# Kernel optimization log

Measured on AMD Instinct MI355X. Metric: run time of the kernel, lower is better.

Reference implementation:

```python
import jax, jax.numpy as jnp
import numpy as np

B, D, L = 4096, 128, 4
ALPHA = 1.0
SLOPE = 0.1  # LeakyReLU negative slope


def _leaky(h):
    return jnp.where(h > 0, h, SLOPE * h)


def _dleaky(h):
    return jnp.where(h > 0, 1.0, SLOPE).astype(h.dtype)


def setup_inputs() -> dict:
    key = jax.random.key(0)
    ks = jax.random.split(key, 7)
    scale = 0.5 / np.sqrt(D)  # keep residual roughly Lipschitz < 1
    x = jax.random.normal(ks[0], (B, D), jnp.float32)
    W1 = jax.random.normal(ks[1], (L, D, D), jnp.float32) * scale
    b1 = jax.random.normal(ks[2], (L, D), jnp.float32) * 0.01
    W2 = jax.random.normal(ks[3], (L, D, D), jnp.float32) * scale
    b2 = jax.random.normal(ks[4], (L, D), jnp.float32) * 0.01
    W3 = jax.random.normal(ks[5], (L, D, D), jnp.float32) * scale
    b3 = jax.random.normal(ks[6], (L, D), jnp.float32) * 0.01
    return {"x": x, "W1": W1, "b1": b1, "W2": W2, "b2": b2, "W3": W3, "b3": b3}


def reference(x, W1, b1, W2, b2, W3, b3):
    logdet = jnp.zeros(x.shape[0], x.dtype)
    for i in range(L):  # small fixed number of structurally distinct blocks
        w1, w2, w3 = W1[i], W2[i], W3[i]
        # --- block forward: x <- x + alpha * f(x) ---
        h1 = x @ w1.T + b1[i]
        h2 = _leaky(h1) @ w2.T + b2[i]
        f = _leaky(h2) @ w3.T + b3[i]
        x = x + ALPHA * f
        # --- log|det J_f| evaluated at the NEW x (as in the original code) ---
        g1 = x @ w1.T + b1[i]          # [B, D] pre-activation 1
        d1 = _dleaky(g1)
        g2 = _leaky(g1) @ w2.T + b2[i]  # [B, D] pre-activation 2
        d2 = _dleaky(g2)
        # J[b] = w3 @ diag(d2[b]) @ w2 @ diag(d1[b]) @ w1  -> [B, D, D]
        J = (w3[None, :, :] * d2[:, None, :]) @ w2
        J = (J * d1[:, None, :]) @ w1
        s = jnp.linalg.svd(J, compute_uv=False)  # [B, D] singular values
        logdet = logdet + jnp.sum(jnp.log(s), axis=-1)
    return x, logdet
```

## Files before the change

### kernel.cpp

```cpp
#include <hip/hip_runtime.h>

typedef __attribute__((ext_vector_type(8))) short short8;
typedef __attribute__((ext_vector_type(4))) float float4f;

#define PITCH 136
#define ROWS 32
#define LOG_SLOPE -2.302585092994046f
#define LN2 0.6931471805599453f
#define NBLK 140
#define LDS_BYTES 69760
#define WS_BIAS 4160
#define WS_WPLANES 8192
#define NWELEM 196608

__device__ __forceinline__ float bf2f(unsigned int u) {
    return __builtin_bit_cast(float, u << 16);
}
__device__ __forceinline__ unsigned short f2bf(float f) {
    unsigned int x = __builtin_bit_cast(unsigned int, f);
    x += 0x7fff + ((x >> 16) & 1);
    return (unsigned short)(x >> 16);
}
__device__ __forceinline__ float4f vmsub(float4f a, float s, float4f b) {
    a[0] -= s * b[0]; a[1] -= s * b[1]; a[2] -= s * b[2]; a[3] -= s * b[3];
    return a;
}

template<int ISF32>
__device__ __forceinline__ float ldv(const void* p, int i) {
    if (ISF32) return ((const float*)p)[i];
    return bf2f(((const unsigned short*)p)[i]);
}

__device__ __forceinline__ int detect_f32(const unsigned short* W1u, int lane) {
    unsigned int u = W1u[lane * 2];
    unsigned int e = (u >> 7) & 0xFF;
    int bad = (e < 64) || (e > 135);
    return __ballot(bad) != 0ull;
}

__device__ __forceinline__ float4f mfma16(short8 a, short8 b, float4f c) {
    return __builtin_amdgcn_mfma_f32_16x16x32_bf16(a, b, c, 0, 0, 0);
}

__device__ __forceinline__ void split8(float4f a, float4f b, short8& hi, short8& lo) {
#pragma unroll
    for (int j = 0; j < 4; ++j) {
        float v = a[j]; unsigned short h = f2bf(v);
        hi[j] = (short)h; lo[j] = (short)f2bf(v - bf2f(h));
        v = b[j]; h = f2bf(v);
        hi[4 + j] = (short)h; lo[4 + j] = (short)f2bf(v - bf2f(h));
    }
}

__global__ void k_prep(const void* __restrict__ W1, const void* __restrict__ W2,
                       const void* __restrict__ W3, const void* __restrict__ b1,
                       const void* __restrict__ b2, const void* __restrict__ b3,
                       float* __restrict__ ws) {
    const int tid = threadIdx.x, bid = blockIdx.x;
    const int isf32 = detect_f32((const unsigned short*)W1, tid & 63);
    unsigned short* whi = (unsigned short*)(ws + WS_WPLANES);
    unsigned short* wlo = whi + NWELEM;
    if (bid < 96) {
        int s = (bid * 256 + tid) * 8;
        int mat = s >> 14, off = s & 16383;
        int wsel = mat >> 2;
        const void* Wm = wsel == 0 ? W1 : (wsel == 1 ? W2 : W3);
        int src = (mat & 3) * 16384 + off;
        short8 hi, lo;
        if (isf32) {
            const float* p = (const float*)Wm + src;
            split8(*(const float4f*)p, *(const float4f*)(p + 4), hi, lo);
        } else {
            hi = *(const short8*)((const unsigned short*)Wm + src);
            lo = (short8){0, 0, 0, 0, 0, 0, 0, 0};
        }
        *(short8*)(whi + s) = hi;
        *(short8*)(wlo + s) = lo;
    } else {
        for (int e = tid; e < 1536; e += 256) {
            int bsel = e >> 9, idx = e & 511;
            const void* bp = bsel == 0 ? b1 : (bsel == 1 ? b2 : b3);
            ws[WS_BIAS + e] = isf32 ? ((const float*)bp)[idx]
                                    : bf2f(((const unsigned short*)bp)[idx]);
        }
        if (tid == 0) ((int*)ws)[0] = 0;
    }
}

struct W8 { short8 v[16]; };

__device__ __forceinline__ W8 loadW(const unsigned short* __restrict__ wh,
                                    const unsigned short* __restrict__ wl,
                                    int c0, int c1, int q) {
    W8 r;
#pragma unroll
    for (int kk = 0; kk < 4; ++kk) {
        const int kc = kk * 32 + q * 8;
        r.v[kk * 4 + 0] = *(const short8*)(wh + c0 * 128 + kc);
        r.v[kk * 4 + 1] = *(const short8*)(wh + c1 * 128 + kc);
        r.v[kk * 4 + 2] = *(const short8*)(wl + c0 * 128 + kc);
        r.v[kk * 4 + 3] = *(const short8*)(wl + c1 * 128 + kc);
    }
    return r;
}

template<int MODE>
__device__ __forceinline__ W8 matvec(const W8& w,
        const unsigned short* inh, const unsigned short* inl,
        unsigned short* outh, unsigned short* outl,
        const unsigned short* resh, const unsigned short* resl,
        const unsigned short* __restrict__ nwh, const unsigned short* __restrict__ nwl,
        const float* __restrict__ bias,
        int lane, int colb, int* cnt) {
    const int m = lane & 15, q = lane >> 4;
    const int c0 = colb + m, c1 = colb + 16 + m;
    float b0 = bias[c0], b1v = bias[c1];
    float4f acc[2][2];
#pragma unroll
    for (int rt = 0; rt < 2; ++rt) {
        acc[rt][0] = (float4f){b0, b0, b0, b0};
        acc[rt][1] = (float4f){b1v, b1v, b1v, b1v};
    }
    __syncthreads();
    W8 wn = loadW(nwh, nwl, c0, c1, q);
#pragma unroll
    for (int kk = 0; kk < 4; ++kk) {
        const int kc = kk * 32 + q * 8;
#pragma unroll
        for (int rt = 0; rt < 2; ++rt) {
            short8 xh = *(const short8*)(inh + (rt * 16 + m) * PITCH + kc);
            short8 xl = *(const short8*)(inl + (rt * 16 + m) * PITCH + kc);
            acc[rt][0] = mfma16(xh, w.v[kk * 4 + 0], acc[rt][0]);
            acc[rt][0] = mfma16(xl, w.v[kk * 4 + 0], acc[rt][0]);
            acc[rt][0] = mfma16(xh, w.v[kk * 4 + 2], acc[rt][0]);
            acc[rt][1] = mfma16(xh, w.v[kk * 4 + 1], acc[rt][1]);
            acc[rt][1] = mfma16(xl, w.v[kk * 4 + 1], acc[rt][1]);
            acc[rt][1] = mfma16(xh, w.v[kk * 4 + 3], acc[rt][1]);
        }
    }
    int c[2][4];
#pragma unroll
    for (int rt = 0; rt < 2; ++rt) {
#pragma unroll
        for (int r = 0; r < 4; ++r) {
            float v0 = acc[rt][0][r], v1 = acc[rt][1][r];
            int row = rt * 16 + q * 4 + r;
            int o0 = row * PITCH + c0, o1 = row * PITCH + c1;
            if (MODE == 1) {
                v0 += bf2f(resh[o0]) + bf2f(resl[o0]);
                v1 += bf2f(resh[o1]) + bf2f(resl[o1]);
            }
            if (MODE >= 2) c[rt][r] = (v0 <= 0.0f) + (v1 <= 0.0f);
            if (MODE == 0 || MODE == 2) {
                v0 = v0 > 0.0f ? v0 : 0.1f * v0;
                v1 = v1 > 0.0f ? v1 : 0.1f * v1;
            }
            if (MODE != 3) {
                unsigned short h0 = f2bf(v0);
                outh[o0] = h0; outl[o0] = f2bf(v0 - bf2f(h0));
                unsigned short h1 = f2bf(v1);
                outh[o1] = h1; outl[o1] = f2bf(v1 - bf2f(h1));
            }
        }
    }
    if (MODE >= 2) {
#pragma unroll
        for (int rt = 0; rt < 2; ++rt) {
#pragma unroll
            for (int r = 0; r < 4; ++r) {
                int cc = c[rt][r];
                cc += __shfl_xor(cc, 1);
                cc += __shfl_xor(cc, 2);
                cc += __shfl_xor(cc, 4);
                cc += __shfl_xor(cc, 8);
                if (m == 0) atomicAdd(&cnt[rt * 16 + q * 4 + r], cc);
            }
        }
    }
    return wn;
}

template<int ISF32>
__device__ __forceinline__ void fwd(int bid, int tid, int lane, char* ldsb,
                                    const void* x, const float* ws, void* out,
                                    float* wsw) {
    unsigned short* P = (unsigned short*)ldsb;
    unsigned short* Ah = P;
    unsigned short* Al = P + 1 * ROWS * PITCH;
    unsigned short* Bh = P + 2 * ROWS * PITCH;
    unsigned short* Bl = P + 3 * ROWS * PITCH;
    unsigned short* Th = P + 4 * ROWS * PITCH;
    unsigned short* Tl = P + 5 * ROWS * PITCH;
    unsigned short* Uh = P + 6 * ROWS * PITCH;
    unsigned short* Ul = P + 7 * ROWS * PITCH;
    int* cnt = (int*)(P + 8 * ROWS * PITCH);
    const unsigned short* whi = (const unsigned short*)(ws + WS_WPLANES);
    const unsigned short* wlo = whi + NWELEM;
    const float* bias = ws + WS_BIAS;
    const int r0 = bid * ROWS;
    const int m = lane & 15, q = lane >> 4;
    const int colb = (tid >> 6) * 32;
    const int c0 = colb + m, c1 = colb + 16 + m;
    W8 wcur = loadW(whi, wlo, c0, c1, q);
    for (int e = tid; e < ROWS * 128; e += 256) {
        int r = e >> 7, c = e & 127;
        float v = ldv<ISF32>(x, (r0 + r) * 128 + c);
        unsigned short h = f2bf(v);
        Ah[r * PITCH + c] = h;
        Al[r * PITCH + c] = f2bf(v - bf2f(h));
    }
    if (tid < ROWS) cnt[tid] = 0;
    unsigned short *curh = Ah, *curl = Al, *othh = Bh, *othl = Bl;
#pragma unroll 1
    for (int layer = 0; layer < 4; ++layer) {
        const unsigned short* w1h = whi + (0 + layer) * 16384;
        const unsigned short* w1l = wlo + (0 + layer) * 16384;
        const unsigned short* w2h = whi + (4 + layer) * 16384;
        const unsigned short* w2l = wlo + (4 + layer) * 16384;
        const unsigned short* w3h = whi + (8 + layer) * 16384;
        const unsigned short* w3l = wlo + (8 + layer) * 16384;
        const unsigned short* n1h = whi + ((layer + 1) & 3) * 16384;
        const unsigned short* n1l = wlo + ((layer + 1) & 3) * 16384;
        const float* b1p = bias + layer * 128;
        const float* b2p = bias + 512 + layer * 128;
        const float* b3p = bias + 1024 + layer * 128;
        wcur = matvec<0>(wcur, curh, curl, Th, Tl, 0, 0, w2h, w2l, b1p, lane, colb, cnt);
        wcur = matvec<0>(wcur, Th, Tl, Uh, Ul, 0, 0, w3h, w3l, b2p, lane, colb, cnt);
        wcur = matvec<1>(wcur, Uh, Ul, othh, othl, curh, curl, w1h, w1l, b3p, lane, colb, cnt);
        wcur = matvec<2>(wcur, othh, othl, Th, Tl, 0, 0, w2h, w2l, b1p, lane, colb, cnt);
        wcur = matvec<3>(wcur, Th, Tl, Th, Tl, 0, 0, n1h, n1l, b2p, lane, colb, cnt);
        unsigned short* t;
        t = curh; curh = othh; othh = t;
        t = curl; curl = othl; othl = t;
    }
    __syncthreads();
    for (int e = tid; e < ROWS * 128; e += 256) {
        int r = e >> 7, c = e & 127;
        float v = bf2f(curh[r * PITCH + c]) + bf2f(curl[r * PITCH + c]);
        if (ISF32) ((float*)out)[(r0 + r) * 128 + c] = v;
        else ((unsigned short*)out)[(r0 + r) * 128 + c] = f2bf(v);
    }
    if (tid < ROWS) wsw[64 + r0 + tid] = (float)cnt[tid];
}

template<int ISF32>
__device__ __forceinline__ float lu_logdet(int id, int tid, float* lds,
        const void* W1, const void* W2, const void* W3) {
    const int wsel = id % 3;
    const void* Wm = (wsel == 0 ? W1 : (wsel == 1 ? W2 : W3));
    const int ofs = (id / 3) * 16384;
    const int tx = tid & 31, ty = tid >> 5;
    float* rowbuf = lds;
    float* colbuf = lds + 1024;
    float4f V[16];
#pragma unroll
    for (int m = 0; m < 16; ++m) {
        int base = ofs + (ty + 8 * m) * 128 + 4 * tx;
        if (ISF32) {
            V[m] = *(const float4f*)((const float*)Wm + base);
        } else {
            ushort4 u = *(const ushort4*)((const unsigned short*)Wm + base);
            V[m] = (float4f){bf2f(u.x), bf2f(u.y), bf2f(u.z), bf2f(u.w)};
        }
    }
    if (ty < 4) *(float4f*)&rowbuf[ty * 128 + 4 * tx] = V[0];
    if (tx == 0) {
#pragma unroll
        for (int j = 0; j < 4; ++j) {
#pragma unroll
            for (int mg = 0; mg < 4; ++mg) {
                float4f t = {V[mg * 4 + 0][j], V[mg * 4 + 1][j],
                             V[mg * 4 + 2][j], V[mg * 4 + 3][j]};
                *(float4f*)&colbuf[j * 128 + ty * 16 + mg * 4] = t;
            }
        }
    }
    __syncthreads();
    float logacc = 0.0f;
#pragma unroll 1
    for (int kap = 0; kap < 32; ++kap) {
        const int K = kap * 4;
        const int buf = (kap & 1) * 512;
        float4f D[4], R[4], C[4][4];
#pragma unroll
        for (int j = 0; j < 4; ++j) {
            D[j] = *(const float4f*)&rowbuf[buf + j * 128 + K];
            R[j] = *(const float4f*)&rowbuf[buf + j * 128 + 4 * tx];
#pragma unroll
            for (int mg = 0; mg < 4; ++mg)
                C[j][mg] = *(const float4f*)&colbuf[buf + j * 128 + ty * 16 + mg * 4];
        }
        float p0 = D[0][0], i0 = 1.0f / p0;
        float l10 = D[1][0] * i0, l20 = D[2][0] * i0, l30 = D[3][0] * i0;
        D[1] = vmsub(D[1], l10, D[0]); R[1] = vmsub(R[1], l10, R[0]);
        D[2] = vmsub(D[2], l20, D[0]); R[2] = vmsub(R[2], l20, R[0]);
        D[3] = vmsub(D[3], l30, D[0]); R[3] = vmsub(R[3], l30, R[0]);
        float p1 = D[1][1], i1 = 1.0f / p1;
        float l21 = D[2][1] * i1, l31 = D[3][1] * i1;
        D[2] = vmsub(D[2], l21, D[1]); R[2] = vmsub(R[2], l21, R[1]);
        D[3] = vmsub(D[3], l31, D[1]); R[3] = vmsub(R[3], l31, R[1]);
        float p2 = D[2][2], i2 = 1.0f / p2;
        float l32 = D[3][2] * i2;
        D[3] = vmsub(D[3], l32, D[2]); R[3] = vmsub(R[3], l32, R[2]);
        float p3 = D[3][3], i3 = 1.0f / p3;
        logacc += __log2f(fabsf(p0)) + __log2f(fabsf(p1))
                + __log2f(fabsf(p2)) + __log2f(fabsf(p3));
        float iv[4] = {i0, i1, i2, i3};
#pragma unroll
        for (int i = 0; i < 4; ++i) {
#pragma unroll
            for (int mg = 0; mg < 4; ++mg) {
#pragma unroll
                for (int e = 0; e < 4; ++e) {
                    int r = ty + 32 * mg + 8 * e;
                    C[i][mg][e] = (r > K + i) ? C[i][mg][e] * iv[i] : 0.0f;
                }
            }
#pragma unroll
            for (int j = i + 1; j < 4; ++j) {
                float uij = D[i][j];
#pragma unroll
                for (int mg = 0; mg < 4; ++mg)
                    C[j][mg] = vmsub(C[j][mg], uij, C[i][mg]);
            }
        }
#pragma unroll
        for (int mg = 0; mg < 4; ++mg) {
#pragma unroll
            for (int e = 0; e < 4; ++e) {
                float4f v = V[mg * 4 + e];
                v = vmsub(v, C[0][mg][e], R[0]);
                v = vmsub(v, C[1][mg][e], R[1]);
                v = vmsub(v, C[2][mg][e], R[2]);
                v = vmsub(v, C[3][mg][e], R[3]);
                V[mg * 4 + e] = v;
            }
        }
        if (kap < 31) {
            const int nbuf = ((kap + 1) & 1) * 512;
            const int tb = (kap & 1) ? 0 : 4;
            const int mn = (kap + 1) >> 1;
            if (ty >= tb && ty < tb + 4) {
                float4f val;
                switch (mn) {
                case 0:  val = V[0];  break; case 1:  val = V[1];  break;
                case 2:  val = V[2];  break; case 3:  val = V[3];  break;
                case 4:  val = V[4];  break; case 5:  val = V[5];  break;
                case 6:  val = V[6];  break; case 7:  val = V[7];  break;
                case 8:  val = V[8];  break; case 9:  val = V[9];  break;
                case 10: val = V[10]; break; case 11: val = V[11]; break;
                case 12: val = V[12]; break; case 13: val = V[13]; break;
                case 14: val = V[14]; break; default: val = V[15]; break;
                }
                *(float4f*)&rowbuf[nbuf + (ty - tb) * 128 + 4 * tx] = val;
            }
            if (tx == kap + 1) {
#pragma unroll
                for (int j = 0; j < 4; ++j) {
#pragma unroll
                    for (int mg = 0; mg < 4; ++mg) {
                        float4f t = {V[mg * 4 + 0][j], V[mg * 4 + 1][j],
                                     V[mg * 4 + 2][j], V[mg * 4 + 3][j]};
                        *(float4f*)&colbuf[nbuf + j * 128 + ty * 16 + mg * 4] = t;
                    }
                }
            }
        }
        __syncthreads();
    }
    return logacc * LN2;
}

__global__ __launch_bounds__(256) void k_main(
        const void* __restrict__ x,
        const void* __restrict__ W1, const void* __restrict__ b1,
        const void* __restrict__ W2, const void* __restrict__ b2,
        const void* __restrict__ W3, const void* __restrict__ b3,
        void* __restrict__ out, float* __restrict__ ws) {
    extern __shared__ __align__(16) char ldsb[];
    __shared__ int s_last;
    const int tid = threadIdx.x;
    const int lane = tid & 63;
    const int isf32 = detect_f32((const unsigned short*)W1, lane);

    if (blockIdx.x < 12) {
        float ld = isf32 ? lu_logdet<1>(blockIdx.x, tid, (float*)ldsb, W1, W2, W3)
                         : lu_logdet<0>(blockIdx.x, tid, (float*)ldsb, W1, W2, W3);
        if (tid == 0) ws[2 + blockIdx.x] = ld;
    } else {
        const int bid = blockIdx.x - 12;
        if (isf32) fwd<1>(bid, tid, lane, ldsb, x, ws, out, ws);
        else       fwd<0>(bid, tid, lane, ldsb, x, ws, out, ws);
    }

    __threadfence();
    if (tid == 0) s_last = (atomicAdd((int*)ws, 1) == NBLK - 1);
    __syncthreads();
    if (!s_last) return;
    __threadfence();
    float s = 0.0f;
#pragma unroll
    for (int i = 0; i < 12; ++i) s += ws[2 + i];
    for (int b = tid; b < 4096; b += 256) {
        float v = s + LOG_SLOPE * ws[64 + b];
        if (isf32) ((float*)out)[524288 + b] = v;
        else ((unsigned short*)out)[524288 + b] = f2bf(v);
    }
}

extern "C" void kernel_launch(void* const* d_in, const int* in_sizes, int n_in,
                              void* d_out, int out_size, void* d_ws, size_t ws_size,
                              hipStream_t stream) {
    const void* x  = d_in[0];
    const void* W1 = d_in[1];
    const void* b1 = d_in[2];
    const void* W2 = d_in[3];
    const void* b2 = d_in[4];
    const void* W3 = d_in[5];
    const void* b3 = d_in[6];
    float* ws = (float*)d_ws;

    hipLaunchKernelGGL(k_prep, dim3(97), dim3(256), 0, stream,
                       W1, W2, W3, b1, b2, b3, ws);
    hipLaunchKernelGGL(k_main, dim3(NBLK), dim3(256), LDS_BYTES, stream,
                       x, W1, b1, W2, b2, W3, b3, d_out, ws);
}
```

Baseline: 136.5 us.

## Fuse weight hi/lo split into main kernel and drop prep kernel

Measured after the change: 147.9 us. 8.3% more time.

```diff
diff --git a/kernel.cpp b/kernel.cpp
--- a/kernel.cpp
+++ b/kernel.cpp
@@ -9,9 +9,6 @@
 #define LN2 0.6931471805599453f
 #define NBLK 140
 #define LDS_BYTES 69760
-#define WS_BIAS 4160
-#define WS_WPLANES 8192
-#define NWELEM 196608
 
 __device__ __forceinline__ float bf2f(unsigned int u) {
     return __builtin_bit_cast(float, u << 16);
@@ -53,69 +50,84 @@
     }
 }
 
-__global__ void k_prep(const void* __restrict__ W1, const void* __restrict__ W2,
-                       const void* __restrict__ W3, const void* __restrict__ b1,
-                       const void* __restrict__ b2, const void* __restrict__ b3,
-                       float* __restrict__ ws) {
-    const int tid = threadIdx.x, bid = blockIdx.x;
-    const int isf32 = detect_f32((const unsigned short*)W1, tid & 63);
-    unsigned short* whi = (unsigned short*)(ws + WS_WPLANES);
-    unsigned short* wlo = whi + NWELEM;
-    if (bid < 96) {
-        int s = (bid * 256 + tid) * 8;
-        int mat = s >> 14, off = s & 16383;
-        int wsel = mat >> 2;
-        const void* Wm = wsel == 0 ? W1 : (wsel == 1 ? W2 : W3);
-        int src = (mat & 3) * 16384 + off;
-        short8 hi, lo;
-        if (isf32) {
-            const float* p = (const float*)Wm + src;
-            split8(*(const float4f*)p, *(const float4f*)(p + 4), hi, lo);
-        } else {
-            hi = *(const short8*)((const unsigned short*)Wm + src);
-            lo = (short8){0, 0, 0, 0, 0, 0, 0, 0};
-        }
-        *(short8*)(whi + s) = hi;
-        *(short8*)(wlo + s) = lo;
-    } else {
-        for (int e = tid; e < 1536; e += 256) {
-            int bsel = e >> 9, idx = e & 511;
-            const void* bp = bsel == 0 ? b1 : (bsel == 1 ? b2 : b3);
-            ws[WS_BIAS + e] = isf32 ? ((const float*)bp)[idx]
-                                    : bf2f(((const unsigned short*)bp)[idx]);
-        }
-        if (tid == 0) ((int*)ws)[0] = 0;
-    }
-}
-
 struct W8 { short8 v[16]; };
-
-__device__ __forceinline__ W8 loadW(const unsigned short* __restrict__ wh,
-                                    const unsigned short* __restrict__ wl,
-                                    int c0, int c1, int q) {
-    W8 r;
+template<int ISF32> struct WRaw;
+template<> struct WRaw<1> { float4f v[16]; };
+template<> struct WRaw<0> { short8 v[8];  };
+
+template<int ISF32>
+__device__ __forceinline__ WRaw<ISF32> loadRaw(const void* W, int c0, int c1, int q);
+template<>
+__device__ __forceinline__ WRaw<1> loadRaw<1>(const void* W, int c0, int c1, int q) {
+    WRaw<1> r;
+    const float* p = (const float*)W;
 #pragma unroll
     for (int kk = 0; kk < 4; ++kk) {
         const int kc = kk * 32 + q * 8;
-        r.v[kk * 4 + 0] = *(const short8*)(wh + c0 * 128 + kc);
-        r.v[kk * 4 + 1] = *(const short8*)(wh + c1 * 128 + kc);
-        r.v[kk * 4 + 2] = *(const short8*)(wl + c0 * 128 + kc);
-        r.v[kk * 4 + 3] = *(const short8*)(wl + c1 * 128 + kc);
+        r.v[kk * 4 + 0] = *(const float4f*)(p + c0 * 128 + kc);
+        r.v[kk * 4 + 1] = *(const float4f*)(p + c0 * 128 + kc + 4);
+        r.v[kk * 4 + 2] = *(const float4f*)(p + c1 * 128 + kc);
+        r.v[kk * 4 + 3] = *(const float4f*)(p + c1 * 128 + kc + 4);
     }
     return r;
 }
-
-template<int MODE>
+template<>
+__device__ __forceinline__ WRaw<0> loadRaw<0>(const void* W, int c0, int c1, int q) {
+    WRaw<0> r;
+    const unsigned short* p = (const unsigned short*)W;
+#pragma unroll
+    for (int kk = 0; kk < 4; ++kk) {
+        const int kc = kk * 32 + q * 8;
+        r.v[kk * 2 + 0] = *(const short8*)(p + c0 * 128 + kc);
+        r.v[kk * 2 + 1] = *(const short8*)(p + c1 * 128 + kc);
+    }
+    return r;
+}
+
+template<int ISF32>
+__device__ __forceinline__ W8 convertW(const WRaw<ISF32>& raw);
+template<>
+__device__ __forceinline__ W8 convertW<1>(const WRaw<1>& raw) {
+    W8 w;
+#pragma unroll
+    for (int kk = 0; kk < 4; ++kk) {
+        split8(raw.v[kk * 4 + 0], raw.v[kk * 4 + 1], w.v[kk * 4 + 0], w.v[kk * 4 + 2]);
+        split8(raw.v[kk * 4 + 2], raw.v[kk * 4 + 3], w.v[kk * 4 + 1], w.v[kk * 4 + 3]);
+    }
+    return w;
+}
+template<>
+__device__ __forceinline__ W8 convertW<0>(const WRaw<0>& raw) {
+    W8 w;
+    const short8 z = {0, 0, 0, 0, 0, 0, 0, 0};
+#pragma unroll
+    for (int kk = 0; kk < 4; ++kk) {
+        w.v[kk * 4 + 0] = raw.v[kk * 2 + 0];
+        w.v[kk * 4 + 1] = raw.v[kk * 2 + 1];
+        w.v[kk * 4 + 2] = z;
+        w.v[kk * 4 + 3] = z;
+    }
+    return w;
+}
+
+template<int ISF32>
+__device__ __forceinline__ const void* wptr(const void* W, int ofs) {
+    return ISF32 ? (const void*)((const float*)W + ofs)
+                 : (const void*)((const unsigned short*)W + ofs);
+}
+
+template<int MODE, int ISF32>
 __device__ __forceinline__ W8 matvec(const W8& w,
         const unsigned short* inh, const unsigned short* inl,
         unsigned short* outh, unsigned short* outl,
         const unsigned short* resh, const unsigned short* resl,
-        const unsigned short* __restrict__ nwh, const unsigned short* __restrict__ nwl,
-        const float* __restrict__ bias,
+        const void* __restrict__ nw,
+        const void* __restrict__ bias, int bofs,
         int lane, int colb, int* cnt) {
     const int m = lane & 15, q = lane >> 4;
     const int c0 = colb + m, c1 = colb + 16 + m;
-    float b0 = bias[c0], b1v = bias[c1];
+    float b0 = ldv<ISF32>(bias, bofs + c0);
+    float b1v = ldv<ISF32>(bias, bofs + c1);
     float4f acc[2][2];
 #pragma unroll
     for (int rt = 0; rt < 2; ++rt) {
@@ -123,7 +135,7 @@
         acc[rt][1] = (float4f){b1v, b1v, b1v, b1v};
     }
     __syncthreads();
-    W8 wn = loadW(nwh, nwl, c0, c1, q);
+    WRaw<ISF32> raw = loadRaw<ISF32>(nw, c0, c1, q);
 #pragma unroll
     for (int kk = 0; kk < 4; ++kk) {
         const int kc = kk * 32 + q * 8;
@@ -139,6 +151,7 @@
             acc[rt][1] = mfma16(xh, w.v[kk * 4 + 3], acc[rt][1]);
         }
     }
+    W8 wn = convertW<ISF32>(raw);
     int c[2][4];
 #pragma unroll
     for (int rt = 0; rt < 2; ++rt) {
@@ -183,8 +196,8 @@
 
 template<int ISF32>
 __device__ __forceinline__ void fwd(int bid, int tid, int lane, char* ldsb,
-                                    const void* x, const float* ws, void* out,
-                                    float* wsw) {
+        const void* x, const void* W1, const void* b1, const void* W2,
+        const void* b2, const void* W3, const void* b3, void* out, float* wsw) {
     unsigned short* P = (unsigned short*)ldsb;
     unsigned short* Ah = P;
     unsigned short* Al = P + 1 * ROWS * PITCH;
@@ -195,14 +208,11 @@
     unsigned short* Uh = P + 6 * ROWS * PITCH;
     unsigned short* Ul = P + 7 * ROWS * PITCH;
     int* cnt = (int*)(P + 8 * ROWS * PITCH);
-    const unsigned short* whi = (const unsigned short*)(ws + WS_WPLANES);
-    const unsigned short* wlo = whi + NWELEM;
-    const float* bias = ws + WS_BIAS;
     const int r0 = bid * ROWS;
     const int m = lane & 15, q = lane >> 4;
     const int colb = (tid >> 6) * 32;
     const int c0 = colb + m, c1 = colb + 16 + m;
-    W8 wcur = loadW(whi, wlo, c0, c1, q);
+    WRaw<ISF32> raw0 = loadRaw<ISF32>(W1, c0, c1, q);
     for (int e = tid; e < ROWS * 128; e += 256) {
         int r = e >> 7, c = e & 127;
         float v = ldv<ISF32>(x, (r0 + r) * 128 + c);
@@ -211,25 +221,20 @@
         Al[r * PITCH + c] = f2bf(v - bf2f(h));
     }
     if (tid < ROWS) cnt[tid] = 0;
+    W8 wcur = convertW<ISF32>(raw0);
     unsigned short *curh = Ah, *curl = Al, *othh = Bh, *othl = Bl;
 #pragma unroll 1
     for (int layer = 0; layer < 4; ++layer) {
-        const unsigned short* w1h = whi + (0 + layer) * 16384;
-        const unsigned short* w1l = wlo + (0 + layer) * 16384;
-        const unsigned short* w2h = whi + (4 + layer) * 16384;
-        const unsigned short* w2l = wlo + (4 + layer) * 16384;
-        const unsigned short* w3h = whi + (8 + layer) * 16384;
-        const unsigned short* w3l = wlo + (8 + layer) * 16384;
-        const unsigned short* n1h = whi + ((layer + 1) & 3) * 16384;
-        const unsigned short* n1l = wlo + ((layer + 1) & 3) * 16384;
-        const float* b1p = bias + layer * 128;
-        const float* b2p = bias + 512 + layer * 128;
-        const float* b3p = bias + 1024 + layer * 128;
-        wcur = matvec<0>(wcur, curh, curl, Th, Tl, 0, 0, w2h, w2l, b1p, lane, colb, cnt);
-        wcur = matvec<0>(wcur, Th, Tl, Uh, Ul, 0, 0, w3h, w3l, b2p, lane, colb, cnt);
-        wcur = matvec<1>(wcur, Uh, Ul, othh, othl, curh, curl, w1h, w1l, b3p, lane, colb, cnt);
-        wcur = matvec<2>(wcur, othh, othl, Th, Tl, 0, 0, w2h, w2l, b1p, lane, colb, cnt);
-        wcur = matvec<3>(wcur, Th, Tl, Th, Tl, 0, 0, n1h, n1l, b2p, lane, colb, cnt);
+        const int wofs = layer * 16384, bofs = layer * 128;
+        const void* w1p = wptr<ISF32>(W1, wofs);
+        const void* w2p = wptr<ISF32>(W2, wofs);
+        const void* w3p = wptr<ISF32>(W3, wofs);
+        const void* n1p = wptr<ISF32>(W1, ((layer + 1) & 3) * 16384);
+        wcur = matvec<0, ISF32>(wcur, curh, curl, Th, Tl, 0, 0, w2p, b1, bofs, lane, colb, cnt);
+        wcur = matvec<0, ISF32>(wcur, Th, Tl, Uh, Ul, 0, 0, w3p, b2, bofs, lane, colb, cnt);
+        wcur = matvec<1, ISF32>(wcur, Uh, Ul, othh, othl, curh, curl, w1p, b3, bofs, lane, colb, cnt);
+        wcur = matvec<2, ISF32>(wcur, othh, othl, Th, Tl, 0, 0, w2p, b1, bofs, lane, colb, cnt);
+        wcur = matvec<3, ISF32>(wcur, Th, Tl, Th, Tl, 0, 0, n1p, b2, bofs, lane, colb, cnt);
         unsigned short* t;
         t = curh; curh = othh; othh = t;
         t = curl; curl = othl; othl = t;
@@ -372,7 +377,7 @@
     return logacc * LN2;
 }
 
-__global__ __launch_bounds__(256) void k_main(
+__global__ __launch_bounds__(256, 1) void k_main(
         const void* __restrict__ x,
         const void* __restrict__ W1, const void* __restrict__ b1,
         const void* __restrict__ W2, const void* __restrict__ b2,
@@ -390,8 +395,8 @@
         if (tid == 0) ws[2 + blockIdx.x] = ld;
     } else {
         const int bid = blockIdx.x - 12;
-        if (isf32) fwd<1>(bid, tid, lane, ldsb, x, ws, out, ws);
-        else       fwd<0>(bid, tid, lane, ldsb, x, ws, out, ws);
+        if (isf32) fwd<1>(bid, tid, lane, ldsb, x, W1, b1, W2, b2, W3, b3, out, ws);
+        else       fwd<0>(bid, tid, lane, ldsb, x, W1, b1, W2, b2, W3, b3, out, ws);
     }
 
     __threadfence();
@@ -421,8 +426,7 @@
     const void* b3 = d_in[6];
     float* ws = (float*)d_ws;
 
-    hipLaunchKernelGGL(k_prep, dim3(97), dim3(256), 0, stream,
-                       W1, W2, W3, b1, b2, b3, ws);
+    hipMemsetAsync(d_ws, 0, 8, stream);
     hipLaunchKernelGGL(k_main, dim3(NBLK), dim3(256), LDS_BYTES, stream,
                        x, W1, b1, W2, b2, W3, b3, d_out, ws);
 }
```

## Widen blocked LU panel from 4 to 8 columns in logdet path

Applied to the files above, without the earlier changes.

Result: slower. 146.2 us (+7.1%).

```diff
diff --git a/kernel.cpp b/kernel.cpp
--- a/kernel.cpp
+++ b/kernel.cpp
@@ -252,7 +252,7 @@
     const int ofs = (id / 3) * 16384;
     const int tx = tid & 31, ty = tid >> 5;
     float* rowbuf = lds;
-    float* colbuf = lds + 1024;
+    float* colbuf = lds + 2048;
     float4f V[16];
 #pragma unroll
     for (int m = 0; m < 16; ++m) {
@@ -264,51 +264,51 @@
             V[m] = (float4f){bf2f(u.x), bf2f(u.y), bf2f(u.z), bf2f(u.w)};
         }
     }
-    if (ty < 4) *(float4f*)&rowbuf[ty * 128 + 4 * tx] = V[0];
-    if (tx == 0) {
-#pragma unroll
-        for (int j = 0; j < 4; ++j) {
+    *(float4f*)&rowbuf[ty * 128 + 4 * tx] = V[0];
+    if (tx < 2) {
+#pragma unroll
+        for (int j0 = 0; j0 < 4; ++j0) {
 #pragma unroll
             for (int mg = 0; mg < 4; ++mg) {
-                float4f t = {V[mg * 4 + 0][j], V[mg * 4 + 1][j],
-                             V[mg * 4 + 2][j], V[mg * 4 + 3][j]};
-                *(float4f*)&colbuf[j * 128 + ty * 16 + mg * 4] = t;
+                float4f t = {V[mg * 4 + 0][j0], V[mg * 4 + 1][j0],
+                             V[mg * 4 + 2][j0], V[mg * 4 + 3][j0]};
+                *(float4f*)&colbuf[(tx * 4 + j0) * 128 + ty * 16 + mg * 4] = t;
             }
         }
     }
     __syncthreads();
     float logacc = 0.0f;
 #pragma unroll 1
-    for (int kap = 0; kap < 32; ++kap) {
-        const int K = kap * 4;
-        const int buf = (kap & 1) * 512;
-        float4f D[4], R[4], C[4][4];
-#pragma unroll
-        for (int j = 0; j < 4; ++j) {
-            D[j] = *(const float4f*)&rowbuf[buf + j * 128 + K];
+    for (int kap = 0; kap < 16; ++kap) {
+        const int K = kap * 8;
+        const int buf = (kap & 1) * 1024;
+        float4f D[8][2], R[8], C[8][4];
+#pragma unroll
+        for (int j = 0; j < 8; ++j) {
+            D[j][0] = *(const float4f*)&rowbuf[buf + j * 128 + K];
+            D[j][1] = *(const float4f*)&rowbuf[buf + j * 128 + K + 4];
             R[j] = *(const float4f*)&rowbuf[buf + j * 128 + 4 * tx];
 #pragma unroll
             for (int mg = 0; mg < 4; ++mg)
                 C[j][mg] = *(const float4f*)&colbuf[buf + j * 128 + ty * 16 + mg * 4];
         }
-        float p0 = D[0][0], i0 = 1.0f / p0;
-        float l10 = D[1][0] * i0, l20 = D[2][0] * i0, l30 = D[3][0] * i0;
-        D[1] = vmsub(D[1], l10, D[0]); R[1] = vmsub(R[1], l10, R[0]);
-        D[2] = vmsub(D[2], l20, D[0]); R[2] = vmsub(R[2], l20, R[0]);
-        D[3] = vmsub(D[3], l30, D[0]); R[3] = vmsub(R[3], l30, R[0]);
-        float p1 = D[1][1], i1 = 1.0f / p1;
-        float l21 = D[2][1] * i1, l31 = D[3][1] * i1;
-        D[2] = vmsub(D[2], l21, D[1]); R[2] = vmsub(R[2], l21, R[1]);
-        D[3] = vmsub(D[3], l31, D[1]); R[3] = vmsub(R[3], l31, R[1]);
-        float p2 = D[2][2], i2 = 1.0f / p2;
-        float l32 = D[3][2] * i2;
-        D[3] = vmsub(D[3], l32, D[2]); R[3] = vmsub(R[3], l32, R[2]);
-        float p3 = D[3][3], i3 = 1.0f / p3;
-        logacc += __log2f(fabsf(p0)) + __log2f(fabsf(p1))
-                + __log2f(fabsf(p2)) + __log2f(fabsf(p3));
-        float iv[4] = {i0, i1, i2, i3};
-#pragma unroll
-        for (int i = 0; i < 4; ++i) {
+        float iv[8];
+#pragma unroll
+        for (int i = 0; i < 8; ++i) {
+            float pi = D[i][i >> 2][i & 3];
+            float ivi = 1.0f / pi;
+            iv[i] = ivi;
+            logacc += __log2f(fabsf(pi));
+#pragma unroll
+            for (int j = i + 1; j < 8; ++j) {
+                float l = D[j][i >> 2][i & 3] * ivi;
+                D[j][0] = vmsub(D[j][0], l, D[i][0]);
+                D[j][1] = vmsub(D[j][1], l, D[i][1]);
+                R[j] = vmsub(R[j], l, R[i]);
+            }
+        }
+#pragma unroll
+        for (int i = 0; i < 8; ++i) {
 #pragma unroll
             for (int mg = 0; mg < 4; ++mg) {
 #pragma unroll
@@ -318,8 +318,8 @@
                 }
             }
 #pragma unroll
-            for (int j = i + 1; j < 4; ++j) {
-                float uij = D[i][j];
+            for (int j = i + 1; j < 8; ++j) {
+                float uij = D[i][j >> 2][j & 3];
 #pragma unroll
                 for (int mg = 0; mg < 4; ++mg)
                     C[j][mg] = vmsub(C[j][mg], uij, C[i][mg]);
@@ -330,39 +330,36 @@
 #pragma unroll
             for (int e = 0; e < 4; ++e) {
                 float4f v = V[mg * 4 + e];
-                v = vmsub(v, C[0][mg][e], R[0]);
-                v = vmsub(v, C[1][mg][e], R[1]);
-                v = vmsub(v, C[2][mg][e], R[2]);
-                v = vmsub(v, C[3][mg][e], R[3]);
+#pragma unroll
+                for (int i = 0; i < 8; ++i)
+                    v = vmsub(v, C[i][mg][e], R[i]);
                 V[mg * 4 + e] = v;
             }
         }
-        if (kap < 31) {
-            const int nbuf = ((kap + 1) & 1) * 512;
-            const int tb = (kap & 1) ? 0 : 4;
-            const int mn = (kap + 1) >> 1;
-            if (ty >= tb && ty < tb + 4) {
-                float4f val;
-                switch (mn) {
-                case 0:  val = V[0];  break; case 1:  val = V[1];  break;
-                case 2:  val = V[2];  break; case 3:  val = V[3];  break;
-                case 4:  val = V[4];  break; case 5:  val = V[5];  break;
-                case 6:  val = V[6];  break; case 7:  val = V[7];  break;
-                case 8:  val = V[8];  break; case 9:  val = V[9];  break;
-                case 10: val = V[10]; break; case 11: val = V[11]; break;
-                case 12: val = V[12]; break; case 13: val = V[13]; break;
-                case 14: val = V[14]; break; default: val = V[15]; break;
-                }
-                *(float4f*)&rowbuf[nbuf + (ty - tb) * 128 + 4 * tx] = val;
-            }
-            if (tx == kap + 1) {
-#pragma unroll
-                for (int j = 0; j < 4; ++j) {
+        if (kap < 15) {
+            const int nbuf = ((kap + 1) & 1) * 1024;
+            float4f val;
+            switch (kap + 1) {
+            case 1:  val = V[1];  break; case 2:  val = V[2];  break;
+            case 3:  val = V[3];  break; case 4:  val = V[4];  break;
+            case 5:  val = V[5];  break; case 6:  val = V[6];  break;
+            case 7:  val = V[7];  break; case 8:  val = V[8];  break;
+            case 9:  val = V[9];  break; case 10: val = V[10]; break;
+            case 11: val = V[11]; break; case 12: val = V[12]; break;
+            case 13: val = V[13]; break; case 14: val = V[14]; break;
+            default: val = V[15]; break;
+            }
+            *(float4f*)&rowbuf[nbuf + ty * 128 + 4 * tx] = val;
+            const int txb = 2 * (kap + 1);
+            if (tx == txb || tx == txb + 1) {
+                const int jb = (tx - txb) * 4;
+#pragma unroll
+                for (int j0 = 0; j0 < 4; ++j0) {
 #pragma unroll
                     for (int mg = 0; mg < 4; ++mg) {
-                        float4f t = {V[mg * 4 + 0][j], V[mg * 4 + 1][j],
-                                     V[mg * 4 + 2][j], V[mg * 4 + 3][j]};
-                        *(float4f*)&colbuf[nbuf + j * 128 + ty * 16 + mg * 4] = t;
+                        float4f t = {V[mg * 4 + 0][j0], V[mg * 4 + 1][j0],
+                                     V[mg * 4 + 2][j0], V[mg * 4 + 3][j0]};
+                        *(float4f*)&colbuf[nbuf + (jb + j0) * 128 + ty * 16 + mg * 4] = t;
                     }
                 }
             }
@@ -372,7 +369,7 @@
     return logacc * LN2;
 }
 
-__global__ __launch_bounds__(256) void k_main(
+__global__ __launch_bounds__(256, 1) void k_main(
         const void* __restrict__ x,
         const void* __restrict__ W1, const void* __restrict__ b1,
         const void* __restrict__ W2, const void* __restrict__ b2,
```

## Double block size to 512 threads, halving per-thread work in matvec and LU

Applied to the files above, without the earlier changes.

After: 140.8 us. 1.03x slower.

```diff
diff --git a/kernel.cpp b/kernel.cpp
--- a/kernel.cpp
+++ b/kernel.cpp
@@ -5,6 +5,7 @@
 
 #define PITCH 136
 #define ROWS 32
+#define THREADS 512
 #define LOG_SLOPE -2.302585092994046f
 #define LN2 0.6931471805599453f
 #define NBLK 140
@@ -88,25 +89,23 @@
     }
 }
 
-struct W8 { short8 v[16]; };
-
-__device__ __forceinline__ W8 loadW(const unsigned short* __restrict__ wh,
-                                    const unsigned short* __restrict__ wl,
-                                    int c0, int c1, int q) {
-    W8 r;
+struct W4 { short8 v[8]; };
+
+__device__ __forceinline__ W4 loadW4(const unsigned short* __restrict__ wh,
+                                     const unsigned short* __restrict__ wl,
+                                     int c0, int q) {
+    W4 r;
 #pragma unroll
     for (int kk = 0; kk < 4; ++kk) {
         const int kc = kk * 32 + q * 8;
-        r.v[kk * 4 + 0] = *(const short8*)(wh + c0 * 128 + kc);
-        r.v[kk * 4 + 1] = *(const short8*)(wh + c1 * 128 + kc);
-        r.v[kk * 4 + 2] = *(const short8*)(wl + c0 * 128 + kc);
-        r.v[kk * 4 + 3] = *(const short8*)(wl + c1 * 128 + kc);
+        r.v[kk * 2 + 0] = *(const short8*)(wh + c0 * 128 + kc);
+        r.v[kk * 2 + 1] = *(const short8*)(wl + c0 * 128 + kc);
     }
     return r;
 }
 
 template<int MODE>
-__device__ __forceinline__ W8 matvec(const W8& w,
+__device__ __forceinline__ W4 matvec(const W4& w,
         const unsigned short* inh, const unsigned short* inl,
         unsigned short* outh, unsigned short* outl,
         const unsigned short* resh, const unsigned short* resl,
@@ -114,53 +113,40 @@
         const float* __restrict__ bias,
         int lane, int colb, int* cnt) {
     const int m = lane & 15, q = lane >> 4;
-    const int c0 = colb + m, c1 = colb + 16 + m;
-    float b0 = bias[c0], b1v = bias[c1];
-    float4f acc[2][2];
-#pragma unroll
-    for (int rt = 0; rt < 2; ++rt) {
-        acc[rt][0] = (float4f){b0, b0, b0, b0};
-        acc[rt][1] = (float4f){b1v, b1v, b1v, b1v};
-    }
+    const int c0 = colb + m;
+    float b0 = bias[c0];
+    float4f acc0 = {b0, b0, b0, b0};
+    float4f acc1 = {b0, b0, b0, b0};
     __syncthreads();
-    W8 wn = loadW(nwh, nwl, c0, c1, q);
+    W4 wn = loadW4(nwh, nwl, c0, q);
 #pragma unroll
     for (int kk = 0; kk < 4; ++kk) {
         const int kc = kk * 32 + q * 8;
-#pragma unroll
-        for (int rt = 0; rt < 2; ++rt) {
-            short8 xh = *(const short8*)(inh + (rt * 16 + m) * PITCH + kc);
-            short8 xl = *(const short8*)(inl + (rt * 16 + m) * PITCH + kc);
-            acc[rt][0] = mfma16(xh, w.v[kk * 4 + 0], acc[rt][0]);
-            acc[rt][0] = mfma16(xl, w.v[kk * 4 + 0], acc[rt][0]);
-            acc[rt][0] = mfma16(xh, w.v[kk * 4 + 2], acc[rt][0]);
-            acc[rt][1] = mfma16(xh, w.v[kk * 4 + 1], acc[rt][1]);
-            acc[rt][1] = mfma16(xl, w.v[kk * 4 + 1], acc[rt][1]);
-            acc[rt][1] = mfma16(xh, w.v[kk * 4 + 3], acc[rt][1]);
-        }
+        short8 x0h = *(const short8*)(inh + m * PITCH + kc);
+        short8 x0l = *(const short8*)(inl + m * PITCH + kc);
+        short8 x1h = *(const short8*)(inh + (16 + m) * PITCH + kc);
+        short8 x1l = *(const short8*)(inl + (16 + m) * PITCH + kc);
+        acc0 = mfma16(x0h, w.v[kk * 2 + 0], acc0);
+        acc0 = mfma16(x0l, w.v[kk * 2 + 0], acc0);
+        acc0 = mfma16(x0h, w.v[kk * 2 + 1], acc0);
+        acc1 = mfma16(x1h, w.v[kk * 2 + 0], acc1);
+        acc1 = mfma16(x1l, w.v[kk * 2 + 0], acc1);
+        acc1 = mfma16(x1h, w.v[kk * 2 + 1], acc1);
     }
     int c[2][4];
 #pragma unroll
     for (int rt = 0; rt < 2; ++rt) {
 #pragma unroll
         for (int r = 0; r < 4; ++r) {
-            float v0 = acc[rt][0][r], v1 = acc[rt][1][r];
+            float v0 = rt == 0 ? acc0[r] : acc1[r];
             int row = rt * 16 + q * 4 + r;
-            int o0 = row * PITCH + c0, o1 = row * PITCH + c1;
-            if (MODE == 1) {
-                v0 += bf2f(resh[o0]) + bf2f(resl[o0]);
-                v1 += bf2f(resh[o1]) + bf2f(resl[o1]);
-            }
-            if (MODE >= 2) c[rt][r] = (v0 <= 0.0f) + (v1 <= 0.0f);
-            if (MODE == 0 || MODE == 2) {
-                v0 = v0 > 0.0f ? v0 : 0.1f * v0;
-                v1 = v1 > 0.0f ? v1 : 0.1f * v1;
-            }
+            int o0 = row * PITCH + c0;
+            if (MODE == 1) v0 += bf2f(resh[o0]) + bf2f(resl[o0]);
+            if (MODE >= 2) c[rt][r] = (v0 <= 0.0f);
+            if (MODE == 0 || MODE == 2) v0 = v0 > 0.0f ? v0 : 0.1f * v0;
             if (MODE != 3) {
                 unsigned short h0 = f2bf(v0);
                 outh[o0] = h0; outl[o0] = f2bf(v0 - bf2f(h0));
-                unsigned short h1 = f2bf(v1);
-                outh[o1] = h1; outl[o1] = f2bf(v1 - bf2f(h1));
             }
         }
     }
@@ -200,10 +186,10 @@
     const float* bias = ws + WS_BIAS;
     const int r0 = bid * ROWS;
     const int m = lane & 15, q = lane >> 4;
-    const int colb = (tid >> 6) * 32;
-    const int c0 = colb + m, c1 = colb + 16 + m;
-    W8 wcur = loadW(whi, wlo, c0, c1, q);
-    for (int e = tid; e < ROWS * 128; e += 256) {
+    const int colb = (tid >> 6) * 16;
+    const int c0 = colb + m;
+    W4 wcur = loadW4(whi, wlo, c0, q);
+    for (int e = tid; e < ROWS * 128; e += THREADS) {
         int r = e >> 7, c = e & 127;
         float v = ldv<ISF32>(x, (r0 + r) * 128 + c);
         unsigned short h = f2bf(v);
@@ -235,7 +221,7 @@
         t = curl; curl = othl; othl = t;
     }
     __syncthreads();
-    for (int e = tid; e < ROWS * 128; e += 256) {
+    for (int e = tid; e < ROWS * 128; e += THREADS) {
         int r = e >> 7, c = e & 127;
         float v = bf2f(curh[r * PITCH + c]) + bf2f(curl[r * PITCH + c]);
         if (ISF32) ((float*)out)[(r0 + r) * 128 + c] = v;
@@ -253,10 +239,10 @@
     const int tx = tid & 31, ty = tid >> 5;
     float* rowbuf = lds;
     float* colbuf = lds + 1024;
-    float4f V[16];
-#pragma unroll
-    for (int m = 0; m < 16; ++m) {
-        int base = ofs + (ty + 8 * m) * 128 + 4 * tx;
+    float4f V[8];
+#pragma unroll
+    for (int m = 0; m < 8; ++m) {
+        int base = ofs + (ty + 16 * m) * 128 + 4 * tx;
         if (ISF32) {
             V[m] = *(const float4f*)((const float*)Wm + base);
         } else {
@@ -268,12 +254,10 @@
     if (tx == 0) {
 #pragma unroll
         for (int j = 0; j < 4; ++j) {
-#pragma unroll
-            for (int mg = 0; mg < 4; ++mg) {
-                float4f t = {V[mg * 4 + 0][j], V[mg * 4 + 1][j],
-                             V[mg * 4 + 2][j], V[mg * 4 + 3][j]};
-                *(float4f*)&colbuf[j * 128 + ty * 16 + mg * 4] = t;
-            }
+            float4f t0 = {V[0][j], V[1][j], V[2][j], V[3][j]};
+            float4f t1 = {V[4][j], V[5][j], V[6][j], V[7][j]};
+            *(float4f*)&colbuf[j * 128 + ty * 8] = t0;
+            *(float4f*)&colbuf[j * 128 + ty * 8 + 4] = t1;
         }
     }
     __syncthreads();
@@ -282,14 +266,13 @@
     for (int kap = 0; kap < 32; ++kap) {
         const int K = kap * 4;
         const int buf = (kap & 1) * 512;
-        float4f D[4], R[4], C[4][4];
+        float4f D[4], R[4], C[4][2];
 #pragma unroll
         for (int j = 0; j < 4; ++j) {
             D[j] = *(const float4f*)&rowbuf[buf + j * 128 + K];
             R[j] = *(const float4f*)&rowbuf[buf + j * 128 + 4 * tx];
-#pragma unroll
-            for (int mg = 0; mg < 4; ++mg)
-                C[j][mg] = *(const float4f*)&colbuf[buf + j * 128 + ty * 16 + mg * 4];
+            C[j][0] = *(const float4f*)&colbuf[buf + j * 128 + ty * 8];
+            C[j][1] = *(const float4f*)&colbuf[buf + j * 128 + ty * 8 + 4];
         }
         float p0 = D[0][0], i0 = 1.0f / p0;
         float l10 = D[1][0] * i0, l20 = D[2][0] * i0, l30 = D[3][0] * i0;
@@ -310,60 +293,49 @@
 #pragma unroll
         for (int i = 0; i < 4; ++i) {
 #pragma unroll
-            for (int mg = 0; mg < 4; ++mg) {
+            for (int cg = 0; cg < 2; ++cg) {
 #pragma unroll
                 for (int e = 0; e < 4; ++e) {
-                    int r = ty + 32 * mg + 8 * e;
-                    C[i][mg][e] = (r > K + i) ? C[i][mg][e] * iv[i] : 0.0f;
+                    int r = ty + 16 * (cg * 4 + e);
+                    C[i][cg][e] = (r > K + i) ? C[i][cg][e] * iv[i] : 0.0f;
                 }
             }
 #pragma unroll
             for (int j = i + 1; j < 4; ++j) {
                 float uij = D[i][j];
-#pragma unroll
-                for (int mg = 0; mg < 4; ++mg)
-                    C[j][mg] = vmsub(C[j][mg], uij, C[i][mg]);
-            }
-        }
-#pragma unroll
-        for (int mg = 0; mg < 4; ++mg) {
-#pragma unroll
-            for (int e = 0; e < 4; ++e) {
-                float4f v = V[mg * 4 + e];
-                v = vmsub(v, C[0][mg][e], R[0]);
-                v = vmsub(v, C[1][mg][e], R[1]);
-                v = vmsub(v, C[2][mg][e], R[2]);
-                v = vmsub(v, C[3][mg][e], R[3]);
-                V[mg * 4 + e] = v;
-            }
+                C[j][0] = vmsub(C[j][0], uij, C[i][0]);
+                C[j][1] = vmsub(C[j][1], uij, C[i][1]);
+            }
+        }
+#pragma unroll
+        for (int m = 0; m < 8; ++m) {
+            float4f v = V[m];
+            v = vmsub(v, C[0][m >> 2][m & 3], R[0]);
+            v = vmsub(v, C[1][m >> 2][m & 3], R[1]);
+            v = vmsub(v, C[2][m >> 2][m & 3], R[2]);
+            v = vmsub(v, C[3][m >> 2][m & 3], R[3]);
+            V[m] = v;
         }
         if (kap < 31) {
+            const int nk = K + 4;
             const int nbuf = ((kap + 1) & 1) * 512;
-            const int tb = (kap & 1) ? 0 : 4;
-            const int mn = (kap + 1) >> 1;
-            if (ty >= tb && ty < tb + 4) {
+            if ((ty >> 2) == ((nk & 15) >> 2)) {
                 float4f val;
-                switch (mn) {
-                case 0:  val = V[0];  break; case 1:  val = V[1];  break;
-                case 2:  val = V[2];  break; case 3:  val = V[3];  break;
-                case 4:  val = V[4];  break; case 5:  val = V[5];  break;
-                case 6:  val = V[6];  break; case 7:  val = V[7];  break;
-                case 8:  val = V[8];  break; case 9:  val = V[9];  break;
-                case 10: val = V[10]; break; case 11: val = V[11]; break;
-                case 12: val = V[12]; break; case 13: val = V[13]; break;
-                case 14: val = V[14]; break; default: val = V[15]; break;
+                switch (nk >> 4) {
+                case 0:  val = V[0]; break; case 1:  val = V[1]; break;
+                case 2:  val = V[2]; break; case 3:  val = V[3]; break;
+                case 4:  val = V[4]; break; case 5:  val = V[5]; break;
+                case 6:  val = V[6]; break; default: val = V[7]; break;
                 }
-                *(float4f*)&rowbuf[nbuf + (ty - tb) * 128 + 4 * tx] = val;
-            }
-            if (tx == kap + 1) {
+                *(float4f*)&rowbuf[nbuf + (ty & 3) * 128 + 4 * tx] = val;
+            }
+            if (tx == (nk >> 2)) {
 #pragma unroll
                 for (int j = 0; j < 4; ++j) {
-#pragma unroll
-                    for (int mg = 0; mg < 4; ++mg) {
-                        float4f t = {V[mg * 4 + 0][j], V[mg * 4 + 1][j],
-                                     V[mg * 4 + 2][j], V[mg * 4 + 3][j]};
-                        *(float4f*)&colbuf[nbuf + j * 128 + ty * 16 + mg * 4] = t;
-                    }
+                    float4f t0 = {V[0][j], V[1][j], V[2][j], V[3][j]};
+                    float4f t1 = {V[4][j], V[5][j], V[6][j], V[7][j]};
+                    *(float4f*)&colbuf[nbuf + j * 128 + ty * 8] = t0;
+                    *(float4f*)&colbuf[nbuf + j * 128 + ty * 8 + 4] = t1;
                 }
             }
         }
@@ -372,7 +344,7 @@
     return logacc * LN2;
 }
 
-__global__ __launch_bounds__(256) void k_main(
+__global__ __launch_bounds__(THREADS, 1) void k_main(
         const void* __restrict__ x,
         const void* __restrict__ W1, const void* __restrict__ b1,
         const void* __restrict__ W2, const void* __restrict__ b2,
@@ -402,7 +374,7 @@
     float s = 0.0f;
 #pragma unroll
     for (int i = 0; i < 12; ++i) s += ws[2 + i];
-    for (int b = tid; b < 4096; b += 256) {
+    for (int b = tid; b < 4096; b += THREADS) {
         float v = s + LOG_SLOPE * ws[64 + b];
         if (isf32) ((float*)out)[524288 + b] = v;
         else ((unsigned short*)out)[524288 + b] = f2bf(v);
@@ -423,6 +395,6 @@
 
     hipLaunchKernelGGL(k_prep, dim3(97), dim3(256), 0, stream,
                        W1, W2, W3, b1, b2, b3, ws);
-    hipLaunchKernelGGL(k_main, dim3(NBLK), dim3(256), LDS_BYTES, stream,
+    hipLaunchKernelGGL(k_main, dim3(NBLK), dim3(THREADS), LDS_BYTES, stream,
                        x, W1, b1, W2, b2, W3, b3, d_out, ws);
 }
```
